# Kernel tuning notes

Hardware: AMD Instinct MI355X
Metric: run time of the kernel (lower is better)

The kernel has to match this reference:

```python
import jax, jax.numpy as jnp
import numpy as np

H = 1024   # hidden_dim
C = 256    # numchars
T = 512    # total_timesteps
LAM = 0.05


def setup_inputs() -> dict:
    key = jax.random.key(0)
    ks = jax.random.split(key, 32)
    s = np.float32(1.0 / np.sqrt(H))
    n = lambda k, shape, sc=s: jax.random.normal(k, shape, dtype=jnp.float32) * sc
    inp = {
        'x': jax.random.uniform(ks[0], (T, C), dtype=jnp.float32),
        # layer 1 state unit (LSTM in=2H) + V: H->C (softmaxed)
        'W_ih_1': n(ks[1], (4 * H, 2 * H)), 'W_hh_1': n(ks[2], (4 * H, H)),
        'b_ih_1': n(ks[3], (4 * H,)), 'b_hh_1': n(ks[4], (4 * H,)),
        'Vw_1': n(ks[5], (C, H)), 'Vb_1': n(ks[6], (C,)),
        # layer 2 state unit (LSTM in=2H) + V: H->H
        'W_ih_2': n(ks[7], (4 * H, 2 * H)), 'W_hh_2': n(ks[8], (4 * H, H)),
        'b_ih_2': n(ks[9], (4 * H,)), 'b_hh_2': n(ks[10], (4 * H,)),
        'Vw_2': n(ks[11], (H, H)), 'Vb_2': n(ks[12], (H,)),
        # layer 3 (top) state unit (LSTM in=H) + V: H->H
        'W_ih_3': n(ks[13], (4 * H, H)), 'W_hh_3': n(ks[14], (4 * H, H)),
        'b_ih_3': n(ks[15], (4 * H,)), 'b_hh_3': n(ks[16], (4 * H,)),
        'Vw_3': n(ks[17], (H, H)), 'Vb_3': n(ks[18], (H,)),
        # error-unit W projections (layers 0..2; top layer's err unit is never run)
        'Ww_0': n(ks[19], (H, C)), 'Wb_0': n(ks[20], (H,)),
        'Ww_1': n(ks[21], (H, H)), 'Wb_1': n(ks[22], (H,)),
        'Ww_2': n(ks[23], (H, H)), 'Wb_2': n(ks[24], (H,)),
        # initial recon vectors (torch init: randn; layer 1 gets softmax in forward)
        'r1': n(ks[25], (C,), 1.0), 'r2': n(ks[26], (H,), 1.0), 'r3': n(ks[27], (H,), 1.0),
        'iternumber': 0,
    }
    return inp


def _lstm_cell(x, h, c, Wih, Whh, bih, bhh):
    g = Wih @ x + bih + Whh @ h + bhh  # [4H], torch gate order i,f,g,o
    i, f, gg, o = jnp.split(g, 4)
    c2 = jax.nn.sigmoid(f) * c + jax.nn.sigmoid(i) * jnp.tanh(gg)
    return jax.nn.sigmoid(o) * jnp.tanh(c2), c2


def reference(x, W_ih_1, W_hh_1, b_ih_1, b_hh_1, Vw_1, Vb_1,
              W_ih_2, W_hh_2, b_ih_2, b_hh_2, Vw_2, Vb_2,
              W_ih_3, W_hh_3, b_ih_3, b_hh_3, Vw_3, Vb_3,
              Ww_0, Wb_0, Ww_1, Wb_1, Ww_2, Wb_2, r1, r2, r3, iternumber):
    zH = jnp.zeros((H,), jnp.float32)

    def step(carry, x_t):
        h1, c1, h2, c2, h3, c3, rec1, rec2, rec3, TD1, TD2, loss, fll = carry
        # lyr 0: state := input char; err unit 0 uses layer-1 recon (previous t)
        s0 = x_t
        u = s0 * jnp.log(rec1) + (1.0 - s0) * jnp.log(1.0 - rec1)
        TD0 = s0 - rec1
        loss0 = -jnp.sum(u)
        BU0 = Ww_0 @ TD0 + Wb_0
        # lyr 1: state unit consumes fresh BU0 and stale TD1, then err unit 1
        h1n, c1n = _lstm_cell(jnp.concatenate([BU0, TD1]), h1, c1, W_ih_1, W_hh_1, b_ih_1, b_hh_1)
        rec1n = jax.nn.softmax(Vw_1 @ h1n + Vb_1)
        TD1n = h1n - rec2
        BU1 = Ww_1 @ TD1n + Wb_1
        # lyr 2
        h2n, c2n = _lstm_cell(jnp.concatenate([BU1, TD2]), h2, c2, W_ih_2, W_hh_2, b_ih_2, b_hh_2)
        rec2n = Vw_2 @ h2n + Vb_2
        TD2n = h2n - rec3
        BU2 = Ww_2 @ TD2n + Wb_2
        # lyr 3 (top): LSTM input is BU2 only; its err unit never runs (TD3 == 0)
        h3n, c3n = _lstm_cell(BU2, h3, c3, W_ih_3, W_hh_3, b_ih_3, b_hh_3)
        rec3n = Vw_3 @ h3n + Vb_3
        loss = loss + loss0 + LAM * jnp.sum(jnp.abs(TD1n)) + (LAM * LAM) * jnp.sum(jnp.abs(TD2n))
        fll = fll + loss0
        new = (h1n, c1n, h2n, c2n, h3n, c3n, rec1n, rec2n, rec3n, TD1n, TD2n, loss, fll)
        return new, rec1n  # prediction at t is layer-1 recon

    init = (zH, zH, zH, zH, zH, zH,
            jax.nn.softmax(r1), r2, r3,  # init recons (layer 1 softmaxed, per init_vars)
            zH, zH, jnp.float32(0.0), jnp.float32(0.0))
    carry, predictions = jax.lax.scan(step, init, x)
    loss, first_layer_loss = carry[-2], carry[-1]
    return loss, first_layer_loss, predictions
```

## Files before the change

### kernel.cpp

```cpp
#include <hip/hip_runtime.h>
#include <math.h>

#define HD 1024
#define CD 256
#define TT 512
#define GD 4096
#define NWG 256
#define NTH 1024
#define WPB 16
#define LAMF 0.05f
#define SMEMB (4 * WPB * HD * 2)

typedef unsigned long long ull;
typedef unsigned short ushortt;
typedef _Float16 hh2 __attribute__((ext_vector_type(2)));

__device__ __align__(16) ushortt hM1[GD * CD];
__device__ __align__(16) ushortt hM2[GD * HD];
__device__ __align__(16) ushortt hM3[GD * HD];
__device__ __align__(16) ushortt hW1b[GD * HD];
__device__ __align__(16) ushortt hWhh1[GD * HD];
__device__ __align__(16) ushortt hW2b[GD * HD];
__device__ __align__(16) ushortt hWhh2[GD * HD];
__device__ __align__(16) ushortt hWhh3[GD * HD];
__device__ __align__(16) ushortt hVw1[CD * HD];
__device__ __align__(16) ushortt hVw2[HD * HD];
__device__ __align__(16) ushortt hVw3[HD * HD];

__device__ __align__(8) ushortt d_h1h[HD], d_TD1h[HD], d_h3h[HD];
__device__ __align__(8) ushortt d_h2h[HD], d_TD2h[HD];
__device__ __align__(16) float d_z1[CD];
__device__ int d_arr[NWG][32];
__device__ int d_rel;

__global__ void pc_init() { d_arr[threadIdx.x][0] = 0; if (threadIdx.x == 0) d_rel = 0; }

__device__ __forceinline__ float sigf(float x)     { return 1.f / (1.f + __expf(-x)); }
__device__ __forceinline__ float tanhfast(float x) { return 1.f - 2.f / (1.f + __expf(2.f * x)); }

__device__ __forceinline__ ushortt f2h(float x) {
  union { ushortt u; _Float16 h; } c; c.h = (_Float16)x; return c.u;
}
__device__ __forceinline__ float h2f(ushortt u) {
  union { ushortt u; _Float16 h; } c; c.u = u; return (float)c.h;
}
__device__ __forceinline__ unsigned packh2(float a, float b) {
  union { unsigned u; hh2 h; } c; c.h = hh2{(_Float16)a, (_Float16)b}; return c.u;
}
__device__ __forceinline__ float fd2(unsigned a, unsigned b, float c) {
  union { unsigned u; hh2 h; } ua, ub; ua.u = a; ub.u = b;
  return __builtin_amdgcn_fdot2(ua.h, ub.h, c, false);
}

__device__ __forceinline__ float cload(const float* p) {
  return __hip_atomic_load(p, __ATOMIC_RELAXED, __HIP_MEMORY_SCOPE_AGENT);
}
__device__ __forceinline__ void cstore(float* p, float v) {
  __hip_atomic_store(p, v, __ATOMIC_RELAXED, __HIP_MEMORY_SCOPE_AGENT);
}
__device__ __forceinline__ float2 cload2(const float* p) {
  union { ull u; float2 f; } c;
  c.u = __hip_atomic_load((const ull*)p, __ATOMIC_RELAXED, __HIP_MEMORY_SCOPE_AGENT);
  return c.f;
}
__device__ __forceinline__ uint2 cloadU2(const ushortt* p) {
  union { ull u; uint2 v; } c;
  c.u = __hip_atomic_load((const ull*)p, __ATOMIC_RELAXED, __HIP_MEMORY_SCOPE_AGENT);
  return c.v;
}
__device__ __forceinline__ void cstoreU2(ushortt* p, uint2 v) {
  union { ull u; uint2 v; } c; c.v = v;
  __hip_atomic_store((ull*)p, c.u, __ATOMIC_RELAXED, __HIP_MEMORY_SCOPE_AGENT);
}

__device__ __forceinline__ void gbar(int& ep) {
  ++ep;
  __syncthreads();
  const int tid = threadIdx.x;
  if (blockIdx.x == 0) {
    if (tid >= 1 && tid < NWG) {
      while (__hip_atomic_load(&d_arr[tid][0], __ATOMIC_RELAXED, __HIP_MEMORY_SCOPE_AGENT) < ep)
        __builtin_amdgcn_s_sleep(1);
    }
    __syncthreads();
    if (tid == 0)
      __hip_atomic_store(&d_rel, ep, __ATOMIC_RELEASE, __HIP_MEMORY_SCOPE_AGENT);
  } else {
    if (tid == 0) {
      __hip_atomic_store(&d_arr[blockIdx.x][0], ep, __ATOMIC_RELEASE, __HIP_MEMORY_SCOPE_AGENT);
      while (__hip_atomic_load(&d_rel, __ATOMIC_RELAXED, __HIP_MEMORY_SCOPE_AGENT) < ep)
        __builtin_amdgcn_s_sleep(1);
    }
    __syncthreads();
  }
}

__device__ __forceinline__ float wredsum(float v) {
  #pragma unroll
  for (int off = 32; off; off >>= 1) v += __shfl_xor(v, off);
  return v;
}
__device__ __forceinline__ float wredmax(float v) {
  #pragma unroll
  for (int off = 32; off; off >>= 1) v = fmaxf(v, __shfl_xor(v, off));
  return v;
}

__device__ __forceinline__ float dotp(const float* __restrict__ w, const float* xv, int n, int lane) {
  float a0 = 0.f, a1 = 0.f, a2 = 0.f, a3 = 0.f;
  for (int c = lane * 4; c < n; c += 256) {
    const float4 wv = *(const float4*)(w + c);
    const float4 vv = *(const float4*)(xv + c);
    a0 = fmaf(wv.x, vv.x, a0); a1 = fmaf(wv.y, vv.y, a1);
    a2 = fmaf(wv.z, vv.z, a2); a3 = fmaf(wv.w, vv.w, a3);
  }
  return (a0 + a1) + (a2 + a3);
}

__device__ __forceinline__ float dotH(const ushortt* __restrict__ w, const ushortt* xv, int lane) {
  const uint4 w0 = *(const uint4*)(w + lane * 8);
  const uint4 w1 = *(const uint4*)(w + lane * 8 + 512);
  const uint4 v0 = *(const uint4*)(xv + lane * 8);
  const uint4 v1 = *(const uint4*)(xv + lane * 8 + 512);
  float a = 0.f;
  a = fd2(w0.x, v0.x, a); a = fd2(w0.y, v0.y, a);
  a = fd2(w0.z, v0.z, a); a = fd2(w0.w, v0.w, a);
  a = fd2(w1.x, v1.x, a); a = fd2(w1.y, v1.y, a);
  a = fd2(w1.z, v1.z, a); a = fd2(w1.w, v1.w, a);
  return a;
}
__device__ __forceinline__ float dotH256(const ushortt* __restrict__ w, const ushortt* xv, int lane) {
  const uint2 wv = *(const uint2*)(w + lane * 4);
  const uint2 vv = *(const uint2*)(xv + lane * 4);
  float a = fd2(wv.x, vv.x, 0.f);
  return fd2(wv.y, vv.y, a);
}

__global__ __launch_bounds__(256) void pc_conv(
    const float* __restrict__ Wih1, const float* __restrict__ Whh1,
    const float* __restrict__ Wih2, const float* __restrict__ Whh2,
    const float* __restrict__ Whh3, const float* __restrict__ Vw1,
    const float* __restrict__ Vw2,  const float* __restrict__ Vw3) {
  const size_t stride = (size_t)gridDim.x * 256;
  const size_t i0 = (size_t)blockIdx.x * 256 + threadIdx.x;
  for (size_t i = i0; i < (size_t)GD * HD; i += stride) {
    size_t r = i >> 10, c = i & 1023;
    size_t src = (r << 11) + HD + c;
    hW1b[i]  = f2h(Wih1[src]);
    hW2b[i]  = f2h(Wih2[src]);
    hWhh1[i] = f2h(Whh1[i]);
    hWhh2[i] = f2h(Whh2[i]);
    hWhh3[i] = f2h(Whh3[i]);
  }
  for (size_t i = i0; i < (size_t)HD * HD; i += stride) {
    hVw2[i] = f2h(Vw2[i]);
    hVw3[i] = f2h(Vw3[i]);
  }
  for (size_t i = i0; i < (size_t)CD * HD; i += stride) hVw1[i] = f2h(Vw1[i]);
}

__global__ __launch_bounds__(256) void pc_fold(
    const float* __restrict__ Wih1, const float* __restrict__ Wih2,
    const float* __restrict__ Wih3, const float* __restrict__ Ww0,
    const float* __restrict__ Ww1,  const float* __restrict__ Ww2) {
  int b = blockIdx.x;
  const float* A; const float* B; ushortt* C; int N, lda;
  if (b < 256)        { A = Wih1; B = Ww0; C = hM1; N = CD; lda = 2 * HD; }
  else if (b < 1280)  { A = Wih2; B = Ww1; C = hM2; N = HD; lda = 2 * HD; b -= 256; }
  else                { A = Wih3; B = Ww2; C = hM3; N = HD; lda = HD;     b -= 1280; }
  const int ctiles = N >> 6;
  const int rt = b / ctiles, ct = b - rt * ctiles;
  const int tid = threadIdx.x;
  const int tx = tid & 15, ty = tid >> 4;

  __shared__ float sA[16][65];
  __shared__ float sB[16][64];

  float acc[4][4] = {};
  const int ar = tid >> 2, aq = tid & 3;
  const int br = tid >> 4, bq = tid & 15;

  for (int kk = 0; kk < HD; kk += 16) {
    float4 av = *(const float4*)(A + (size_t)(rt * 64 + ar) * lda + kk + aq * 4);
    float4 bv = *(const float4*)(B + (size_t)(kk + br) * N + ct * 64 + bq * 4);
    __syncthreads();
    sA[aq * 4 + 0][ar] = av.x; sA[aq * 4 + 1][ar] = av.y;
    sA[aq * 4 + 2][ar] = av.z; sA[aq * 4 + 3][ar] = av.w;
    *(float4*)&sB[br][bq * 4] = bv;
    __syncthreads();
    #pragma unroll
    for (int k = 0; k < 16; ++k) {
      const float4 b4 = *(const float4*)&sB[k][tx * 4];
      const float a0 = sA[k][ty * 4 + 0], a1 = sA[k][ty * 4 + 1];
      const float a2 = sA[k][ty * 4 + 2], a3 = sA[k][ty * 4 + 3];
      acc[0][0] = fmaf(a0, b4.x, acc[0][0]); acc[0][1] = fmaf(a0, b4.y, acc[0][1]);
      acc[0][2] = fmaf(a0, b4.z, acc[0][2]); acc[0][3] = fmaf(a0, b4.w, acc[0][3]);
      acc[1][0] = fmaf(a1, b4.x, acc[1][0]); acc[1][1] = fmaf(a1, b4.y, acc[1][1]);
      acc[1][2] = fmaf(a1, b4.z, acc[1][2]); acc[1][3] = fmaf(a1, b4.w, acc[1][3]);
      acc[2][0] = fmaf(a2, b4.x, acc[2][0]); acc[2][1] = fmaf(a2, b4.y, acc[2][1]);
      acc[2][2] = fmaf(a2, b4.z, acc[2][2]); acc[2][3] = fmaf(a2, b4.w, acc[2][3]);
      acc[3][0] = fmaf(a3, b4.x, acc[3][0]); acc[3][1] = fmaf(a3, b4.y, acc[3][1]);
      acc[3][2] = fmaf(a3, b4.z, acc[3][2]); acc[3][3] = fmaf(a3, b4.w, acc[3][3]);
    }
  }
  #pragma unroll
  for (int i = 0; i < 4; ++i) {
    uint2 r = make_uint2(packh2(acc[i][0], acc[i][1]), packh2(acc[i][2], acc[i][3]));
    *(uint2*)(C + (size_t)(rt * 64 + ty * 4 + i) * N + ct * 64 + tx * 4) = r;
  }
}

__global__ __launch_bounds__(NTH, 1) void pc_main(
    const float* __restrict__ x,
    const float* __restrict__ Wih1, const float* __restrict__ Whh1,
    const float* __restrict__ bih1, const float* __restrict__ bhh1,
    const float* __restrict__ Vw1,  const float* __restrict__ Vb1,
    const float* __restrict__ Wih2, const float* __restrict__ Whh2,
    const float* __restrict__ bih2, const float* __restrict__ bhh2,
    const float* __restrict__ Vw2,  const float* __restrict__ Vb2,
    const float* __restrict__ Wih3, const float* __restrict__ Whh3,
    const float* __restrict__ bih3, const float* __restrict__ bhh3,
    const float* __restrict__ Vw3,  const float* __restrict__ Vb3,
    const float* __restrict__ Ww0,  const float* __restrict__ Wb0,
    const float* __restrict__ Ww1,  const float* __restrict__ Wb1,
    const float* __restrict__ Ww2,  const float* __restrict__ Wb2,
    const float* __restrict__ r1,   const float* __restrict__ r2,
    const float* __restrict__ r3,
    float* __restrict__ out) {
  const int tid  = threadIdx.x;
  const int lane = tid & 63;
  const int bid  = blockIdx.x;
  const int wv   = tid >> 6;
  const int gi   = wv & 3;
  const int slot = wv >> 2;
  const int rg   = gi * HD + bid * 4 + slot;
  const int jown = bid * 4 + slot;
  const bool iswg0 = (bid == 0);
  const bool w0    = iswg0 && tid < 64;

  extern __shared__ __align__(16) ushortt smem[];
  ushortt* sM2 = smem;
  ushortt* sW2 = sM2 + WPB * HD;
  ushortt* sH2 = sW2 + WPB * HD;
  ushortt* sM3 = sH2 + WPB * HD;

  __shared__ __align__(16) ushortt s_TD1[HD], s_h1[HD], s_TD2[HD], s_h2[HD], s_h3[HD];
  __shared__ __align__(16) ushortt s_small[CD];
  __shared__ float s_gateA[WPB], s_gateB[WPB], s_rec[4];
  __shared__ float s_c1own[4], s_c2own[4], s_c3own[4];
  __shared__ __align__(16) float s_ftmp[HD];

  int ep = 0;
  float loss_acc = 0.f, fll_acc = 0.f;
  float b1, b2, b3, vbR3 = 0.f, vbR2 = 0.f, vbZ = 0.f;
  float part1 = 0.f, part2 = 0.f, part3 = 0.f;

  {
    const uint4* gM2 = (const uint4*)(hM2   + (size_t)rg * HD);
    const uint4* gW2 = (const uint4*)(hW2b  + (size_t)rg * HD);
    const uint4* gH2 = (const uint4*)(hWhh2 + (size_t)rg * HD);
    const uint4* gM3 = (const uint4*)(hM3   + (size_t)rg * HD);
    uint4* lM2 = (uint4*)(sM2 + wv * HD);
    uint4* lW2 = (uint4*)(sW2 + wv * HD);
    uint4* lH2 = (uint4*)(sH2 + wv * HD);
    uint4* lM3 = (uint4*)(sM3 + wv * HD);
    #pragma unroll
    for (int i = 0; i < 2; ++i) {
      lM2[lane + 64 * i] = gM2[lane + 64 * i];
      lW2[lane + 64 * i] = gW2[lane + 64 * i];
      lH2[lane + 64 * i] = gH2[lane + 64 * i];
      lM3[lane + 64 * i] = gM3[lane + 64 * i];
    }
  }
  if (tid < 512) *(float2*)(s_ftmp + tid * 2) = *(const float2*)(Wb0 + tid * 2);
  __syncthreads();
  b1 = bih1[rg] + bhh1[rg] + wredsum(dotp(Wih1 + (size_t)rg * 2 * HD, s_ftmp, HD, lane));
  __syncthreads();
  if (tid < 512) *(float2*)(s_ftmp + tid * 2) = *(const float2*)(Wb1 + tid * 2);
  __syncthreads();
  b2 = bih2[rg] + bhh2[rg] + wredsum(dotp(Wih2 + (size_t)rg * 2 * HD, s_ftmp, HD, lane));
  __syncthreads();
  if (tid < 512) *(float2*)(s_ftmp + tid * 2) = *(const float2*)(Wb2 + tid * 2);
  __syncthreads();
  b3 = bih3[rg] + bhh3[rg] + wredsum(dotp(Wih3 + (size_t)rg * HD, s_ftmp, HD, lane));
  if (gi == 0) vbR3 = Vb3[jown];
  if (gi == 2) vbR2 = Vb2[jown];
  if (wv == 1) vbZ  = Vb1[bid];
  if (tid < 4) { s_c2own[tid] = 0.f; s_c3own[tid] = 0.f; }
  if (tid == 0) {
    uint2 z2 = make_uint2(0u, 0u);
    cstoreU2(d_h2h + bid * 4, z2);
    cstoreU2(d_TD2h + bid * 4, z2);
    cstoreU2(d_h3h + bid * 4, z2);
  }
  if (tid < 64) {
    float4 z4 = *(const float4*)(r1 + tid * 4);
    float m = wredmax(fmaxf(fmaxf(z4.x, z4.y), fmaxf(z4.z, z4.w)));
    float e0 = __expf(z4.x - m), e1 = __expf(z4.y - m);
    float e2 = __expf(z4.z - m), e3 = __expf(z4.w - m);
    float inv = 1.f / wredsum((e0 + e1) + (e2 + e3));
    float p0 = e0 * inv, p1 = e1 * inv, p2 = e2 * inv, p3 = e3 * inv;
    float4 xv = *(const float4*)(x + tid * 4);
    *(uint2*)(s_small + tid * 4) =
        make_uint2(packh2(xv.x - p0, xv.y - p1), packh2(xv.z - p2, xv.w - p3));
    if (iswg0) {
      float u = xv.x * __logf(p0) + (1.f - xv.x) * __logf(1.f - p0)
              + xv.y * __logf(p1) + (1.f - xv.y) * __logf(1.f - p1)
              + xv.z * __logf(p2) + (1.f - xv.z) * __logf(1.f - p2)
              + xv.w * __logf(p3) + (1.f - xv.w) * __logf(1.f - p3);
      u = wredsum(u);
      if (tid == 0) { loss_acc -= u; fll_acc -= u; }
    }
  }
  __syncthreads();
  {
    float s = wredsum(dotH256(hM1 + (size_t)rg * CD, s_small, lane)) + b1;
    if (lane == 0) s_gateA[wv] = s;
  }
  __syncthreads();
  if (tid < 64) {
    float h = 0.f, td = 0.f;
    if (lane < 4) {
      float gI = s_gateA[lane * 4 + 0];
      float gG = s_gateA[lane * 4 + 2], gO = s_gateA[lane * 4 + 3];
      float cn = sigf(gI) * tanhfast(gG);
      h  = sigf(gO) * tanhfast(cn);
      td = h - r2[bid * 4 + lane];
      s_c1own[lane] = cn;
    }
    uint2 uh, ut;
    uh.x = packh2(__shfl(h, 0), __shfl(h, 1));  uh.y = packh2(__shfl(h, 2), __shfl(h, 3));
    ut.x = packh2(__shfl(td, 0), __shfl(td, 1)); ut.y = packh2(__shfl(td, 2), __shfl(td, 3));
    if (lane == 0) { cstoreU2(d_h1h + bid * 4, uh); cstoreU2(d_TD1h + bid * 4, ut); }
  }
  part2 = 0.f;
  gbar(ep);

  for (int t = 0; t < TT; ++t) {
    {
      const int grp = tid >> 8, k = tid & 255;
      if (grp == 0)      *(uint2*)(s_TD1 + k * 4) = cloadU2(d_TD1h + k * 4);
      else if (grp == 1) *(uint2*)(s_h1 + k * 4)  = cloadU2(d_h1h + k * 4);
      else if (grp == 2) *(uint2*)(s_h3 + k * 4)  = cloadU2(d_h3h + k * 4);
      __syncthreads();
      if (w0) {
        float a = 0.f;
        #pragma unroll
        for (int kk = 0; kk < 16; ++kk) a += fabsf(h2f(s_TD1[tid + 64 * kk]));
        a = wredsum(a);
        if (tid == 0) loss_acc += LAMF * a;
      }
      {
        float s = wredsum(dotH(sM2 + wv * HD, s_TD1, lane)) + part2 + b2;
        if (lane == 0) s_gateA[wv] = s;
      }
      if (gi == 0) {
        if (t > 0) {
          float s = wredsum(dotH(hVw3 + (size_t)jown * HD, s_h3, lane)) + vbR3;
          if (lane == 0) s_rec[slot] = s;
        } else if (lane == 0) s_rec[slot] = r3[jown];
      }
      if (wv == 1) {
        float s = wredsum(dotH(hVw1 + (size_t)bid * HD, s_h1, lane)) + vbZ;
        if (lane == 0) cstore(&d_z1[bid], s);
      }
      __syncthreads();
      if (tid < 64) {
        float h = 0.f, td = 0.f;
        if (lane < 4) {
          float gI = s_gateA[lane * 4 + 0], gF = s_gateA[lane * 4 + 1];
          float gG = s_gateA[lane * 4 + 2], gO = s_gateA[lane * 4 + 3];
          float cn = sigf(gF) * s_c2own[lane] + sigf(gI) * tanhfast(gG);
          h  = sigf(gO) * tanhfast(cn);
          td = h - s_rec[lane];
          s_c2own[lane] = cn;
        }
        uint2 uh, ut;
        uh.x = packh2(__shfl(h, 0), __shfl(h, 1));  uh.y = packh2(__shfl(h, 2), __shfl(h, 3));
        ut.x = packh2(__shfl(td, 0), __shfl(td, 1)); ut.y = packh2(__shfl(td, 2), __shfl(td, 3));
        if (lane == 0) { cstoreU2(d_h2h + bid * 4, uh); cstoreU2(d_TD2h + bid * 4, ut); }
      }
      part3 = wredsum(dotH(hWhh3 + (size_t)rg * HD, s_h3, lane));
      part1 = wredsum(dotH(hW1b  + (size_t)rg * HD, s_TD1, lane)
                    + dotH(hWhh1 + (size_t)rg * HD, s_h1,  lane));
    }
    gbar(ep);

    {
      const int grp = tid >> 8, k = tid & 255;
      if (grp == 0)      *(uint2*)(s_TD2 + k * 4) = cloadU2(d_TD2h + k * 4);
      else if (grp == 1) *(uint2*)(s_h2 + k * 4)  = cloadU2(d_h2h + k * 4);
      if (tid < 64) {
        float2 za = cload2(&d_z1[tid * 4]), zb = cload2(&d_z1[tid * 4 + 2]);
        float m = wredmax(fmaxf(fmaxf(za.x, za.y), fmaxf(zb.x, zb.y)));
        float e0 = __expf(za.x - m), e1 = __expf(za.y - m);
        float e2 = __expf(zb.x - m), e3 = __expf(zb.y - m);
        float inv = 1.f / wredsum((e0 + e1) + (e2 + e3));
        float p0 = e0 * inv, p1 = e1 * inv, p2 = e2 * inv, p3 = e3 * inv;
        if (t < TT - 1) {
          float4 xv = *(const float4*)(x + (size_t)(t + 1) * CD + tid * 4);
          *(uint2*)(s_small + tid * 4) =
              make_uint2(packh2(xv.x - p0, xv.y - p1), packh2(xv.z - p2, xv.w - p3));
          if (iswg0) {
            float u = xv.x * __logf(p0) + (1.f - xv.x) * __logf(1.f - p0)
                    + xv.y * __logf(p1) + (1.f - xv.y) * __logf(1.f - p1)
                    + xv.z * __logf(p2) + (1.f - xv.z) * __logf(1.f - p2)
                    + xv.w * __logf(p3) + (1.f - xv.w) * __logf(1.f - p3);
            u = wredsum(u);
            if (tid == 0) { loss_acc -= u; fll_acc -= u; }
          }
        }
        if (iswg0) {
          float* po = out + 2 + (size_t)t * CD + tid * 4;
          po[0] = p0; po[1] = p1; po[2] = p2; po[3] = p3;
        }
      }
      __syncthreads();
      if (w0) {
        float a = 0.f;
        #pragma unroll
        for (int kk = 0; kk < 16; ++kk) a += fabsf(h2f(s_TD2[tid + 64 * kk]));
        a = wredsum(a);
        if (tid == 0) loss_acc += (LAMF * LAMF) * a;
      }
      if (t < TT - 1) {
        {
          float s = wredsum(dotH(sM3 + wv * HD, s_TD2, lane)) + part3 + b3;
          if (lane == 0) s_gateB[wv] = s;
        }
        {
          float s = wredsum(dotH256(hM1 + (size_t)rg * CD, s_small, lane)) + part1 + b1;
          if (lane == 0) s_gateA[wv] = s;
        }
        if (gi == 2) {
          float s = wredsum(dotH(hVw2 + (size_t)jown * HD, s_h2, lane)) + vbR2;
          if (lane == 0) s_rec[slot] = s;
        }
        __syncthreads();
        if (tid < 64) {
          float h3n = 0.f, h1n = 0.f, td1 = 0.f;
          if (lane < 4) {
            {
              float gI = s_gateB[lane * 4 + 0], gF = s_gateB[lane * 4 + 1];
              float gG = s_gateB[lane * 4 + 2], gO = s_gateB[lane * 4 + 3];
              float cn = sigf(gF) * s_c3own[lane] + sigf(gI) * tanhfast(gG);
              h3n = sigf(gO) * tanhfast(cn);
              s_c3own[lane] = cn;
            }
            {
              float gI = s_gateA[lane * 4 + 0], gF = s_gateA[lane * 4 + 1];
              float gG = s_gateA[lane * 4 + 2], gO = s_gateA[lane * 4 + 3];
              float cn = sigf(gF) * s_c1own[lane] + sigf(gI) * tanhfast(gG);
              h1n = sigf(gO) * tanhfast(cn);
              td1 = h1n - s_rec[lane];
              s_c1own[lane] = cn;
            }
          }
          uint2 u3, u1, utd;
          u3.x = packh2(__shfl(h3n, 0), __shfl(h3n, 1)); u3.y = packh2(__shfl(h3n, 2), __shfl(h3n, 3));
          u1.x = packh2(__shfl(h1n, 0), __shfl(h1n, 1)); u1.y = packh2(__shfl(h1n, 2), __shfl(h1n, 3));
          utd.x = packh2(__shfl(td1, 0), __shfl(td1, 1)); utd.y = packh2(__shfl(td1, 2), __shfl(td1, 3));
          if (lane == 0) {
            cstoreU2(d_h3h + bid * 4, u3);
            cstoreU2(d_h1h + bid * 4, u1);
            cstoreU2(d_TD1h + bid * 4, utd);
          }
        }
        part2 = wredsum(dotH(sW2 + wv * HD, s_TD2, lane)
                      + dotH(sH2 + wv * HD, s_h2,  lane));
        gbar(ep);
      }
    }
  }

  if (iswg0 && tid == 0) { out[0] = loss_acc; out[1] = fll_acc; }
}

extern "C" void kernel_launch(void* const* d_in, const int* in_sizes, int n_in,
                              void* d_out, int out_size, void* d_ws, size_t ws_size,
                              hipStream_t stream) {
  const float* x    = (const float*)d_in[0];
  const float* Wih1 = (const float*)d_in[1];
  const float* Whh1 = (const float*)d_in[2];
  const float* bih1 = (const float*)d_in[3];
  const float* bhh1 = (const float*)d_in[4];
  const float* Vw1  = (const float*)d_in[5];
  const float* Vb1  = (const float*)d_in[6];
  const float* Wih2 = (const float*)d_in[7];
  const float* Whh2 = (const float*)d_in[8];
  const float* bih2 = (const float*)d_in[9];
  const float* bhh2 = (const float*)d_in[10];
  const float* Vw2  = (const float*)d_in[11];
  const float* Vb2  = (const float*)d_in[12];
  const float* Wih3 = (const float*)d_in[13];
  const float* Whh3 = (const float*)d_in[14];
  const float* bih3 = (const float*)d_in[15];
  const float* bhh3 = (const float*)d_in[16];
  const float* Vw3  = (const float*)d_in[17];
  const float* Vb3  = (const float*)d_in[18];
  const float* Ww0  = (const float*)d_in[19];
  const float* Wb0  = (const float*)d_in[20];
  const float* Ww1  = (const float*)d_in[21];
  const float* Wb1  = (const float*)d_in[22];
  const float* Ww2  = (const float*)d_in[23];
  const float* Wb2  = (const float*)d_in[24];
  const float* r1   = (const float*)d_in[25];
  const float* r2   = (const float*)d_in[26];
  const float* r3   = (const float*)d_in[27];

  static int smem_set = 0;
  if (!smem_set) {
    hipFuncSetAttribute((const void*)pc_main,
                        hipFuncAttributeMaxDynamicSharedMemorySize, SMEMB);
    smem_set = 1;
  }

  pc_conv<<<1024, 256, 0, stream>>>(Wih1, Whh1, Wih2, Whh2, Whh3, Vw1, Vw2, Vw3);
  pc_fold<<<2304, 256, 0, stream>>>(Wih1, Wih2, Wih3, Ww0, Ww1, Ww2);
  pc_init<<<1, NWG, 0, stream>>>();
  pc_main<<<NWG, NTH, SMEMB, stream>>>(x, Wih1, Whh1, bih1, bhh1, Vw1, Vb1,
                                       Wih2, Whh2, bih2, bhh2, Vw2, Vb2,
                                       Wih3, Whh3, bih3, bhh3, Vw3, Vb3,
                                       Ww0, Wb0, Ww1, Wb1, Ww2, Wb2,
                                       r1, r2, r3, (float*)d_out);
}
```

Measured before the change: 7.664 ms.

## Replicate shared state vectors and barrier release flag across eight mirrors

Each producer now writes its slice of h/TD/z1 to eight replicated global buffers, and the barrier release flag is likewise replicated. Each workgroup reads and polls the copy chosen by blockIdx mod 8. The aim is to spread the 256-workgroup polling and broadcast reads across separate cache lines, and possibly separate L2 channels or XCDs, so no single hot line is contended. The cost is eight times more small stores per step and extra release stores in the barrier.

```diff
diff --git a/kernel.cpp b/kernel.cpp
--- a/kernel.cpp
+++ b/kernel.cpp
@@ -8,6 +8,7 @@
 #define NWG 256
 #define NTH 1024
 #define WPB 16
+#define NMIR 8
 #define LAMF 0.05f
 #define SMEMB (4 * WPB * HD * 2)
 
@@ -27,13 +28,16 @@
 __device__ __align__(16) ushortt hVw2[HD * HD];
 __device__ __align__(16) ushortt hVw3[HD * HD];
 
-__device__ __align__(8) ushortt d_h1h[HD], d_TD1h[HD], d_h3h[HD];
-__device__ __align__(8) ushortt d_h2h[HD], d_TD2h[HD];
-__device__ __align__(16) float d_z1[CD];
+__device__ __align__(8) ushortt d_h1m[NMIR][HD], d_TD1m[NMIR][HD], d_h3m[NMIR][HD];
+__device__ __align__(8) ushortt d_h2m[NMIR][HD], d_TD2m[NMIR][HD];
+__device__ __align__(16) float d_z1m[NMIR][CD];
 __device__ int d_arr[NWG][32];
-__device__ int d_rel;
-
-__global__ void pc_init() { d_arr[threadIdx.x][0] = 0; if (threadIdx.x == 0) d_rel = 0; }
+__device__ int d_relm[NMIR][32];
+
+__global__ void pc_init() {
+  d_arr[threadIdx.x][0] = 0;
+  if (threadIdx.x < NMIR) d_relm[threadIdx.x][0] = 0;
+}
 
 __device__ __forceinline__ float sigf(float x)     { return 1.f / (1.f + __expf(-x)); }
 __device__ __forceinline__ float tanhfast(float x) { return 1.f - 2.f / (1.f + __expf(2.f * x)); }
@@ -83,12 +87,13 @@
         __builtin_amdgcn_s_sleep(1);
     }
     __syncthreads();
-    if (tid == 0)
-      __hip_atomic_store(&d_rel, ep, __ATOMIC_RELEASE, __HIP_MEMORY_SCOPE_AGENT);
+    if (tid < NMIR)
+      __hip_atomic_store(&d_relm[tid][0], ep, __ATOMIC_RELEASE, __HIP_MEMORY_SCOPE_AGENT);
   } else {
     if (tid == 0) {
       __hip_atomic_store(&d_arr[blockIdx.x][0], ep, __ATOMIC_RELEASE, __HIP_MEMORY_SCOPE_AGENT);
-      while (__hip_atomic_load(&d_rel, __ATOMIC_RELAXED, __HIP_MEMORY_SCOPE_AGENT) < ep)
+      while (__hip_atomic_load(&d_relm[blockIdx.x & (NMIR - 1)][0],
+                               __ATOMIC_RELAXED, __HIP_MEMORY_SCOPE_AGENT) < ep)
         __builtin_amdgcn_s_sleep(1);
     }
     __syncthreads();
@@ -235,6 +240,7 @@
   const int slot = wv >> 2;
   const int rg   = gi * HD + bid * 4 + slot;
   const int jown = bid * 4 + slot;
+  const int mi   = bid & (NMIR - 1);
   const bool iswg0 = (bid == 0);
   const bool w0    = iswg0 && tid < 64;
 
@@ -287,11 +293,11 @@
   if (gi == 2) vbR2 = Vb2[jown];
   if (wv == 1) vbZ  = Vb1[bid];
   if (tid < 4) { s_c2own[tid] = 0.f; s_c3own[tid] = 0.f; }
-  if (tid == 0) {
+  if (tid < NMIR) {
     uint2 z2 = make_uint2(0u, 0u);
-    cstoreU2(d_h2h + bid * 4, z2);
-    cstoreU2(d_TD2h + bid * 4, z2);
-    cstoreU2(d_h3h + bid * 4, z2);
+    cstoreU2(d_h2m[tid] + bid * 4, z2);
+    cstoreU2(d_TD2m[tid] + bid * 4, z2);
+    cstoreU2(d_h3m[tid] + bid * 4, z2);
   }
   if (tid < 64) {
     float4 z4 = *(const float4*)(r1 + tid * 4);
@@ -331,7 +337,7 @@
     uint2 uh, ut;
     uh.x = packh2(__shfl(h, 0), __shfl(h, 1));  uh.y = packh2(__shfl(h, 2), __shfl(h, 3));
     ut.x = packh2(__shfl(td, 0), __shfl(td, 1)); ut.y = packh2(__shfl(td, 2), __shfl(td, 3));
-    if (lane == 0) { cstoreU2(d_h1h + bid * 4, uh); cstoreU2(d_TD1h + bid * 4, ut); }
+    if (lane < NMIR) { cstoreU2(d_h1m[lane] + bid * 4, uh); cstoreU2(d_TD1m[lane] + bid * 4, ut); }
   }
   part2 = 0.f;
   gbar(ep);
@@ -339,9 +345,9 @@
   for (int t = 0; t < TT; ++t) {
     {
       const int grp = tid >> 8, k = tid & 255;
-      if (grp == 0)      *(uint2*)(s_TD1 + k * 4) = cloadU2(d_TD1h + k * 4);
-      else if (grp == 1) *(uint2*)(s_h1 + k * 4)  = cloadU2(d_h1h + k * 4);
-      else if (grp == 2) *(uint2*)(s_h3 + k * 4)  = cloadU2(d_h3h + k * 4);
+      if (grp == 0)      *(uint2*)(s_TD1 + k * 4) = cloadU2(d_TD1m[mi] + k * 4);
+      else if (grp == 1) *(uint2*)(s_h1 + k * 4)  = cloadU2(d_h1m[mi] + k * 4);
+      else if (grp == 2) *(uint2*)(s_h3 + k * 4)  = cloadU2(d_h3m[mi] + k * 4);
       __syncthreads();
       if (w0) {
         float a = 0.f;
@@ -362,7 +368,7 @@
       }
       if (wv == 1) {
         float s = wredsum(dotH(hVw1 + (size_t)bid * HD, s_h1, lane)) + vbZ;
-        if (lane == 0) cstore(&d_z1[bid], s);
+        if (lane < NMIR) cstore(&d_z1m[lane][bid], s);
       }
       __syncthreads();
       if (tid < 64) {
@@ -378,7 +384,7 @@
         uint2 uh, ut;
         uh.x = packh2(__shfl(h, 0), __shfl(h, 1));  uh.y = packh2(__shfl(h, 2), __shfl(h, 3));
         ut.x = packh2(__shfl(td, 0), __shfl(td, 1)); ut.y = packh2(__shfl(td, 2), __shfl(td, 3));
-        if (lane == 0) { cstoreU2(d_h2h + bid * 4, uh); cstoreU2(d_TD2h + bid * 4, ut); }
+        if (lane < NMIR) { cstoreU2(d_h2m[lane] + bid * 4, uh); cstoreU2(d_TD2m[lane] + bid * 4, ut); }
       }
       part3 = wredsum(dotH(hWhh3 + (size_t)rg * HD, s_h3, lane));
       part1 = wredsum(dotH(hW1b  + (size_t)rg * HD, s_TD1, lane)
@@ -388,10 +394,10 @@
 
     {
       const int grp = tid >> 8, k = tid & 255;
-      if (grp == 0)      *(uint2*)(s_TD2 + k * 4) = cloadU2(d_TD2h + k * 4);
-      else if (grp == 1) *(uint2*)(s_h2 + k * 4)  = cloadU2(d_h2h + k * 4);
+      if (grp == 0)      *(uint2*)(s_TD2 + k * 4) = cloadU2(d_TD2m[mi] + k * 4);
+      else if (grp == 1) *(uint2*)(s_h2 + k * 4)  = cloadU2(d_h2m[mi] + k * 4);
       if (tid < 64) {
-        float2 za = cload2(&d_z1[tid * 4]), zb = cload2(&d_z1[tid * 4 + 2]);
+        float2 za = cload2(&d_z1m[mi][tid * 4]), zb = cload2(&d_z1m[mi][tid * 4 + 2]);
         float m = wredmax(fmaxf(fmaxf(za.x, za.y), fmaxf(zb.x, zb.y)));
         float e0 = __expf(za.x - m), e1 = __expf(za.y - m);
         float e2 = __expf(zb.x - m), e3 = __expf(zb.y - m);
@@ -460,10 +466,10 @@
           u3.x = packh2(__shfl(h3n, 0), __shfl(h3n, 1)); u3.y = packh2(__shfl(h3n, 2), __shfl(h3n, 3));
           u1.x = packh2(__shfl(h1n, 0), __shfl(h1n, 1)); u1.y = packh2(__shfl(h1n, 2), __shfl(h1n, 3));
           utd.x = packh2(__shfl(td1, 0), __shfl(td1, 1)); utd.y = packh2(__shfl(td1, 2), __shfl(td1, 3));
-          if (lane == 0) {
-            cstoreU2(d_h3h + bid * 4, u3);
-            cstoreU2(d_h1h + bid * 4, u1);
-            cstoreU2(d_TD1h + bid * 4, utd);
+          if (lane < NMIR) {
+            cstoreU2(d_h3m[lane] + bid * 4, u3);
+            cstoreU2(d_h1m[lane] + bid * 4, u1);
+            cstoreU2(d_TD1m[lane] + bid * 4, utd);
           }
         }
         part2 = wredsum(dotH(sW2 + wv * HD, s_TD2, lane)
```

Measured after the change: 8.075 ms. +5.4%, slower.
